# Performance work log

Hardware: AMD Instinct MI355X
Metric: run time of the kernel (lower is better)

## Reference

```python
import jax, jax.numpy as jnp
import numpy as np
from jax import lax

NEG = -10000.0
B, L, D = 256, 1024, 126  # batch, doc_len, d_output (tags); padded tagset T = D + 2


def setup_inputs() -> dict:
    key = jax.random.key(0)
    k1, k2, k3, k4 = jax.random.split(key, 4)
    x = jax.random.normal(k1, (B, L, D), dtype=jnp.float32)
    transitions = jax.random.normal(k2, (D + 2, D + 2), dtype=jnp.float32)
    x_len = jax.random.randint(k3, (B,), 1, L + 1, dtype=jnp.int32)
    x_mask = (jnp.arange(L)[None, :] < x_len[:, None]).astype(jnp.float32)
    true_tag = jax.random.randint(k4, (B, L), 0, D, dtype=jnp.int32)
    return {"x": x, "transitions": transitions, "x_mask": x_mask,
            "x_len": x_len, "true_tag": true_tag}


def _loglikelihood(x, transitions, x_mask, x_len, true_tag):
    b, l, d = x.shape
    T = transitions.shape[0]
    START, STOP = T - 2, T - 1
    # pad emissions with two impossible tags (START/STOP)
    logits = jnp.concatenate([x, jnp.full((b, l, 2), NEG, x.dtype)], axis=2)  # [B,L,T]

    # ---- partition function (forward algorithm, log-sum-exp scan) ----
    alpha0 = jnp.full((b, T), NEG, x.dtype).at[:, START].set(0.0)

    def step(alpha, inp):
        logit, m = inp  # [B,T], [B]
        # mat[b,i,j] = trans[i,j] + alpha[b,j] + logit[b,i]
        mat = transitions[None, :, :] + alpha[:, None, :] + logit[:, :, None]
        new = jax.nn.logsumexp(mat, axis=2)  # [B,T]
        m = m[:, None]
        return m * new + (1.0 - m) * alpha, None

    alpha, _ = lax.scan(step, alpha0, (jnp.swapaxes(logits, 0, 1), x_mask.T))
    partition = jax.nn.logsumexp(alpha + transitions[STOP][None, :], axis=1)  # [B]

    # ---- gold sequence score ----
    tag = true_tag.astype(jnp.int32)
    emission = jnp.take_along_axis(logits, tag[:, :, None], axis=2)[:, :, 0]
    emission = jnp.sum(emission * x_mask, axis=1)  # [B]

    tran = transitions[tag[:, 0], START]  # START -> first tag
    pair = transitions[tag[:, 1:], tag[:, :-1]] * x_mask[:, 1:]  # trans[next, prev]
    tran = tran + jnp.sum(pair, axis=1)
    last_tag = jnp.take_along_axis(tag, (x_len.astype(jnp.int32) - 1)[:, None], axis=1)[:, 0]
    tran = tran + transitions[STOP, last_tag]

    return tran + emission - partition  # [B]


def reference(x, transitions, x_mask, x_len, true_tag):
    return _loglikelihood(x, transitions, x_mask, x_len, true_tag)
```

## Files before the change

### kernel.cpp

```cpp
#include <hip/hip_runtime.h>


typedef float v2f __attribute__((ext_vector_type(2)));

#define NEGV  (-10000.0f)
#define LOG2E 1.4426950408889634f
#define LN2   0.6931471805599453f

constexpr int Bc = 256, Lc = 1024, Dc = 126, Tc = 128;

#if __has_builtin(__builtin_amdgcn_exp2f)
#define FEXP2(x) __builtin_amdgcn_exp2f(x)
#else
#define FEXP2(x) exp2f(x)
#endif
#if __has_builtin(__builtin_amdgcn_logf)
#define FLOG2(x) __builtin_amdgcn_logf(x)
#else
#define FLOG2(x) log2f(x)
#endif

#if __has_builtin(__builtin_amdgcn_mov_dpp)
#define DPPF(x, ctrl) __int_as_float(__builtin_amdgcn_mov_dpp(__float_as_int(x), (ctrl), 0xF, 0xF, true))
#define ROR1(x) DPPF(x, 0x121)
#define ROR2(x) DPPF(x, 0x122)
#define ROR4(x) DPPF(x, 0x124)
#define ROR8(x) DPPF(x, 0x128)
#else
#define ROR1(x) __shfl_xor((x), 1, 64)
#define ROR2(x) __shfl_xor((x), 2, 64)
#define ROR4(x) __shfl_xor((x), 4, 64)
#define ROR8(x) __shfl_xor((x), 8, 64)
#endif

#define STEP_BARRIER() asm volatile("s_waitcnt lgkmcnt(0)\n\ts_barrier" ::: "memory")

__device__ __forceinline__ int SIG(int q) { return q ^ (q >> 3); }
__device__ __forceinline__ int Fmap(int k) { return 4 * SIG(k >> 2) + (k & 3); }

__global__ __launch_bounds__(512, 1) void crf_fwd_kernel(
    const float* __restrict__ x,
    const float* __restrict__ trans,
    const int*   __restrict__ x_len,
    const int*   __restrict__ tag,
    float*       __restrict__ out)
{
    __shared__ __align__(16) float E[2][Tc];
    __shared__ float red[12];

    const int b   = blockIdx.x;
    const int tid = threadIdx.x;
    const int w   = tid >> 6;
    const int l6  = tid & 63;
    const int o   = l6 & 15;
    const int jg  = (w << 2) | (l6 >> 4);
    const int len = x_len[b];

    const float* xb = x   + (size_t)b * Lc * Dc;
    const int*   tb = tag + (size_t)b * Lc;

    const int  f0 = 4 * SIG(2 * o);
    const int  f1 = 4 * SIG(2 * o + 1);
    const int  wq = 4 * SIG(jg);
    const bool hiBad = (jg == 31);

    float treg[4][8];
#pragma unroll
    for (int g = 0; g < 4; ++g) {
        const float4* tp = reinterpret_cast<const float4*>(trans + (4*jg + g) * Tc + 8*o);
        float4 t0 = tp[0], t1 = tp[1];
        treg[g][0] = FEXP2(t0.x * LOG2E); treg[g][1] = FEXP2(t0.y * LOG2E);
        treg[g][2] = FEXP2(t0.z * LOG2E); treg[g][3] = FEXP2(t0.w * LOG2E);
        treg[g][4] = FEXP2(t1.x * LOG2E); treg[g][5] = FEXP2(t1.y * LOG2E);
        treg[g][6] = FEXP2(t1.z * LOG2E); treg[g][7] = FEXP2(t1.w * LOG2E);
    }

    if (tid < Tc) E[0][Fmap(tid)] = (tid == Tc - 2) ? 1.0f : 0.0f;
    __syncthreads();

#define LOADP(LS, A, B2) {                                              \
        int _s = (LS); if (_s > len - 1) _s = len - 1;                  \
        const float* _r = xb + (size_t)_s * Dc + 4 * jg;                \
        A  = *reinterpret_cast<const v2f*>(_r);                         \
        B2 = hiBad ? (v2f){NEGV, NEGV}                                  \
                   : *reinterpret_cast<const v2f*>(_r + 2); }

    v2f Pa, Pb;
    {
        v2f a, b2; LOADP(0, a, b2);
        Pa = (v2f){FEXP2(a.x * LOG2E),  FEXP2(a.y * LOG2E)};
        Pb = (v2f){FEXP2(b2.x * LOG2E), FEXP2(b2.y * LOG2E)};
    }
    v2f pA0, pB0, pA1, pB1, pA2, pB2, pA3, pB3;
    LOADP(1, pA1, pB1); LOADP(2, pA2, pB2); LOADP(3, pA3, pB3);
    pA0 = pA1; pB0 = pB1;

    int Mint = 0;
    const int len4 = (len + 3) & ~3;

#define BODY(C, PA_LD, PB_LD, PA_NX, PB_NX) {                                   \
        const int  l   = l4 + (C);                                              \
        const bool act = l < len;                 \
        const int  p   = (C) & 1;                                               \
        LOADP(l + 4, PA_LD, PB_LD);           \
        const float* Ep = E[p];                                                 \
        float4 ea = *reinterpret_cast<const float4*>(Ep + f0);                  \
        float4 eb = *reinterpret_cast<const float4*>(Ep + f1);                  \
        float a0 = treg[0][0]*ea.x, a1 = treg[1][0]*ea.x,                       \
              a2 = treg[2][0]*ea.x, a3 = treg[3][0]*ea.x;                       \
        a0=fmaf(treg[0][1],ea.y,a0); a1=fmaf(treg[1][1],ea.y,a1);               \
        a2=fmaf(treg[2][1],ea.y,a2); a3=fmaf(treg[3][1],ea.y,a3);               \
        a0=fmaf(treg[0][2],ea.z,a0); a1=fmaf(treg[1][2],ea.z,a1);               \
        a2=fmaf(treg[2][2],ea.z,a2); a3=fmaf(treg[3][2],ea.z,a3);               \
        a0=fmaf(treg[0][3],ea.w,a0); a1=fmaf(treg[1][3],ea.w,a1);               \
        a2=fmaf(treg[2][3],ea.w,a2); a3=fmaf(treg[3][3],ea.w,a3);               \
        a0=fmaf(treg[0][4],eb.x,a0); a1=fmaf(treg[1][4],eb.x,a1);               \
        a2=fmaf(treg[2][4],eb.x,a2); a3=fmaf(treg[3][4],eb.x,a3);               \
        a0=fmaf(treg[0][5],eb.y,a0); a1=fmaf(treg[1][5],eb.y,a1);               \
        a2=fmaf(treg[2][5],eb.y,a2); a3=fmaf(treg[3][5],eb.y,a3);               \
        a0=fmaf(treg[0][6],eb.z,a0); a1=fmaf(treg[1][6],eb.z,a1);               \
        a2=fmaf(treg[2][6],eb.z,a2); a3=fmaf(treg[3][6],eb.z,a3);               \
        a0=fmaf(treg[0][7],eb.w,a0); a1=fmaf(treg[1][7],eb.w,a1);               \
        a2=fmaf(treg[2][7],eb.w,a2); a3=fmaf(treg[3][7],eb.w,a3);               \
        a0 += ROR1(a0); a1 += ROR1(a1); a2 += ROR1(a2); a3 += ROR1(a3);         \
        a0 += ROR2(a0); a1 += ROR2(a1); a2 += ROR2(a2); a3 += ROR2(a3);         \
        a0 += ROR4(a0); a1 += ROR4(a1); a2 += ROR4(a2); a3 += ROR4(a3);         \
        a0 += ROR8(a0); a1 += ROR8(a1); a2 += ROR8(a2); a3 += ROR8(a3);         \
        float R = 1.0f;                                                         \
        if ((C) == 3 && act) {               \
            float mx = fmaxf(ea.z, eb.z);                                       \
            mx = fmaxf(mx, ROR1(mx)); mx = fmaxf(mx, ROR2(mx));                 \
            mx = fmaxf(mx, ROR4(mx)); mx = fmaxf(mx, ROR8(mx));                 \
            int ebq = (__float_as_int(mx) >> 23) & 0xFF;                        \
            R = __int_as_float((254 - ebq) << 23);                              \
            Mint += ebq - 127;                                                  \
        }                                                                       \
        if (act && o == 0)                 \
            *reinterpret_cast<float4*>(&E[p ^ 1][wq]) =                         \
                make_float4(a0 * Pa.x * R, a1 * Pa.y * R,                       \
                            a2 * Pb.x * R, a3 * Pb.y * R);                      \
        Pa = (v2f){FEXP2(PA_NX.x * LOG2E), FEXP2(PA_NX.y * LOG2E)};             \
        Pb = (v2f){FEXP2(PB_NX.x * LOG2E), FEXP2(PB_NX.y * LOG2E)};             \
        STEP_BARRIER();                                                         \
    }

    for (int l4 = 0; l4 < len4; l4 += 4) {
        BODY(0, pA0, pB0, pA1, pB1)
        BODY(1, pA1, pB1, pA2, pB2)
        BODY(2, pA2, pB2, pA3, pB3)
        BODY(3, pA3, pB3, pA0, pB0)
    }
#undef BODY
#undef LOADP
    const int pf = len & 1;

    float acc = 0.f;
    for (int l = tid; l < len; l += 512) {
        int   tg = tb[l];
        float tr = (l == 0) ? trans[tg * Tc + (Tc - 2)]
                            : trans[tg * Tc + tb[l - 1]];
        acc += xb[(size_t)l * Dc + tg] + tr;
    }
#pragma unroll
    for (int off = 1; off < 64; off <<= 1)
        acc += __shfl_xor(acc, off, 64);
    if (l6 == 0) red[w] = acc;

    if (w == 0) {
        int k0i = l6, k1i = 64 + l6;
        float p0 = FEXP2(trans[(Tc-1) * Tc + k0i] * LOG2E) * E[pf][Fmap(k0i)];
        float p1 = FEXP2(trans[(Tc-1) * Tc + k1i] * LOG2E) * E[pf][Fmap(k1i)];
        float ps = p0 + p1;
#pragma unroll
        for (int off = 1; off < 64; off <<= 1)
            ps += __shfl_xor(ps, off, 64);
        if (l6 == 0) red[8] = LN2 * ((float)Mint + FLOG2(ps));
    }
    __syncthreads();

    if (tid == 0) {
        float sc = trans[(Tc-1) * Tc + tb[len - 1]];
#pragma unroll
        for (int i = 0; i < 8; ++i) sc += red[i];
        out[b] = sc - red[8];
    }
}

extern "C" void kernel_launch(void* const* d_in, const int* in_sizes, int n_in,
                              void* d_out, int out_size, void* d_ws, size_t ws_size,
                              hipStream_t stream) {
    const float* x     = (const float*)d_in[0];
    const float* trans = (const float*)d_in[1];
    const int*   x_len = (const int*)d_in[3];
    const int*   tag   = (const int*)d_in[4];
    float*       out   = (float*)d_out;

    crf_fwd_kernel<<<Bc, 512, 0, stream>>>(x, trans, x_len, tag, out);
}
```

Measured before the change: 545.4 us.

## Process two batch sequences per block to share barriers and halve grid

Each block now runs the forward recursion for two batch elements at once, interleaving their matrix-vector products, ring reductions and emission loads so a single barrier per step serves both. The goal is to amortise the per-step barrier and LDS latency, which dominate the serial recurrence, across twice the independent work. The grid drops to 128 blocks, fewer than the CU count on MI355X, and each block iterates up to the longer of its two lengths, so idle CUs and length imbalance could offset the gain.

New measurement: 864.4 us. +58.5%, slower.

```diff
diff --git a/kernel.cpp b/kernel.cpp
--- a/kernel.cpp
+++ b/kernel.cpp
@@ -45,19 +45,23 @@
     const int*   __restrict__ tag,
     float*       __restrict__ out)
 {
-    __shared__ __align__(16) float E[2][Tc];
-    __shared__ float red[12];
-
-    const int b   = blockIdx.x;
+    __shared__ __align__(16) float EL[2][2][Tc];
+    __shared__ float red[2][12];
+
+    const int bb  = blockIdx.x << 1;
     const int tid = threadIdx.x;
     const int w   = tid >> 6;
     const int l6  = tid & 63;
     const int o   = l6 & 15;
     const int jg  = (w << 2) | (l6 >> 4);
-    const int len = x_len[b];
-
-    const float* xb = x   + (size_t)b * Lc * Dc;
-    const int*   tb = tag + (size_t)b * Lc;
+    const int len0 = x_len[bb];
+    const int len1 = x_len[bb + 1];
+    const int lenmax = (len0 > len1) ? len0 : len1;
+
+    const float* xb0 = x + (size_t)bb * Lc * Dc;
+    const float* xb1 = xb0 + (size_t)Lc * Dc;
+    const int*   tb0 = tag + (size_t)bb * Lc;
+    const int*   tb1 = tb0 + Lc;
 
     const int  f0 = 4 * SIG(2 * o);
     const int  f1 = 4 * SIG(2 * o + 1);
@@ -75,114 +79,163 @@
         treg[g][6] = FEXP2(t1.z * LOG2E); treg[g][7] = FEXP2(t1.w * LOG2E);
     }
 
-    if (tid < Tc) E[0][Fmap(tid)] = (tid == Tc - 2) ? 1.0f : 0.0f;
+    if (tid < Tc) {
+        float v = (tid == Tc - 2) ? 1.0f : 0.0f;
+        EL[0][0][Fmap(tid)] = v;
+        EL[1][0][Fmap(tid)] = v;
+    }
     __syncthreads();
 
-#define LOADP(LS, A, B2) {                                              \
-        int _s = (LS); if (_s > len - 1) _s = len - 1;                  \
-        const float* _r = xb + (size_t)_s * Dc + 4 * jg;                \
+#define LOADP(Q, LS, A, B2) {                                           \
+        int _s = (LS); const int _lm = len##Q - 1; if (_s > _lm) _s = _lm; \
+        const float* _r = xb##Q + (size_t)_s * Dc + 4 * jg;             \
         A  = *reinterpret_cast<const v2f*>(_r);                         \
         B2 = hiBad ? (v2f){NEGV, NEGV}                                  \
                    : *reinterpret_cast<const v2f*>(_r + 2); }
 
-    v2f Pa, Pb;
+    v2f Pa0, Pb0, Pa1, Pb1;
     {
-        v2f a, b2; LOADP(0, a, b2);
-        Pa = (v2f){FEXP2(a.x * LOG2E),  FEXP2(a.y * LOG2E)};
-        Pb = (v2f){FEXP2(b2.x * LOG2E), FEXP2(b2.y * LOG2E)};
-    }
-    v2f pA0, pB0, pA1, pB1, pA2, pB2, pA3, pB3;
-    LOADP(1, pA1, pB1); LOADP(2, pA2, pB2); LOADP(3, pA3, pB3);
-    pA0 = pA1; pB0 = pB1;
-
-    int Mint = 0;
-    const int len4 = (len + 3) & ~3;
-
-#define BODY(C, PA_LD, PB_LD, PA_NX, PB_NX) {                                   \
-        const int  l   = l4 + (C);                                              \
-        const bool act = l < len;                 \
-        const int  p   = (C) & 1;                                               \
-        LOADP(l + 4, PA_LD, PB_LD);           \
-        const float* Ep = E[p];                                                 \
-        float4 ea = *reinterpret_cast<const float4*>(Ep + f0);                  \
-        float4 eb = *reinterpret_cast<const float4*>(Ep + f1);                  \
-        float a0 = treg[0][0]*ea.x, a1 = treg[1][0]*ea.x,                       \
-              a2 = treg[2][0]*ea.x, a3 = treg[3][0]*ea.x;                       \
-        a0=fmaf(treg[0][1],ea.y,a0); a1=fmaf(treg[1][1],ea.y,a1);               \
-        a2=fmaf(treg[2][1],ea.y,a2); a3=fmaf(treg[3][1],ea.y,a3);               \
-        a0=fmaf(treg[0][2],ea.z,a0); a1=fmaf(treg[1][2],ea.z,a1);               \
-        a2=fmaf(treg[2][2],ea.z,a2); a3=fmaf(treg[3][2],ea.z,a3);               \
-        a0=fmaf(treg[0][3],ea.w,a0); a1=fmaf(treg[1][3],ea.w,a1);               \
-        a2=fmaf(treg[2][3],ea.w,a2); a3=fmaf(treg[3][3],ea.w,a3);               \
-        a0=fmaf(treg[0][4],eb.x,a0); a1=fmaf(treg[1][4],eb.x,a1);               \
-        a2=fmaf(treg[2][4],eb.x,a2); a3=fmaf(treg[3][4],eb.x,a3);               \
-        a0=fmaf(treg[0][5],eb.y,a0); a1=fmaf(treg[1][5],eb.y,a1);               \
-        a2=fmaf(treg[2][5],eb.y,a2); a3=fmaf(treg[3][5],eb.y,a3);               \
-        a0=fmaf(treg[0][6],eb.z,a0); a1=fmaf(treg[1][6],eb.z,a1);               \
-        a2=fmaf(treg[2][6],eb.z,a2); a3=fmaf(treg[3][6],eb.z,a3);               \
-        a0=fmaf(treg[0][7],eb.w,a0); a1=fmaf(treg[1][7],eb.w,a1);               \
-        a2=fmaf(treg[2][7],eb.w,a2); a3=fmaf(treg[3][7],eb.w,a3);               \
-        a0 += ROR1(a0); a1 += ROR1(a1); a2 += ROR1(a2); a3 += ROR1(a3);         \
-        a0 += ROR2(a0); a1 += ROR2(a1); a2 += ROR2(a2); a3 += ROR2(a3);         \
-        a0 += ROR4(a0); a1 += ROR4(a1); a2 += ROR4(a2); a3 += ROR4(a3);         \
-        a0 += ROR8(a0); a1 += ROR8(a1); a2 += ROR8(a2); a3 += ROR8(a3);         \
-        float R = 1.0f;                                                         \
-        if ((C) == 3 && act) {               \
-            float mx = fmaxf(ea.z, eb.z);                                       \
-            mx = fmaxf(mx, ROR1(mx)); mx = fmaxf(mx, ROR2(mx));                 \
-            mx = fmaxf(mx, ROR4(mx)); mx = fmaxf(mx, ROR8(mx));                 \
-            int ebq = (__float_as_int(mx) >> 23) & 0xFF;                        \
-            R = __int_as_float((254 - ebq) << 23);                              \
-            Mint += ebq - 127;                                                  \
+        v2f a, b2;
+        LOADP(0, 0, a, b2);
+        Pa0 = (v2f){FEXP2(a.x * LOG2E),  FEXP2(a.y * LOG2E)};
+        Pb0 = (v2f){FEXP2(b2.x * LOG2E), FEXP2(b2.y * LOG2E)};
+        LOADP(1, 0, a, b2);
+        Pa1 = (v2f){FEXP2(a.x * LOG2E),  FEXP2(a.y * LOG2E)};
+        Pb1 = (v2f){FEXP2(b2.x * LOG2E), FEXP2(b2.y * LOG2E)};
+    }
+    v2f s0A0,s0B0,s0A1,s0B1, s1A0,s1B0,s1A1,s1B1,
+        s2A0,s2B0,s2A1,s2B1, s3A0,s3B0,s3A1,s3B1;
+    LOADP(0, 1, s1A0, s1B0); LOADP(1, 1, s1A1, s1B1);
+    LOADP(0, 2, s2A0, s2B0); LOADP(1, 2, s2A1, s2B1);
+    LOADP(0, 3, s3A0, s3B0); LOADP(1, 3, s3A1, s3B1);
+    s0A0 = s1A0; s0B0 = s1B0; s0A1 = s1A1; s0B1 = s1B1;
+
+    int Mint0 = 0, Mint1 = 0;
+    const int len4 = (lenmax + 3) & ~3;
+
+#define MV32(ea, eb, S0, S1, S2, S3)                                                      \
+    S0 = treg[0][0]*ea.x; S1 = treg[1][0]*ea.x; S2 = treg[2][0]*ea.x; S3 = treg[3][0]*ea.x; \
+    S0=fmaf(treg[0][1],ea.y,S0); S1=fmaf(treg[1][1],ea.y,S1); S2=fmaf(treg[2][1],ea.y,S2); S3=fmaf(treg[3][1],ea.y,S3); \
+    S0=fmaf(treg[0][2],ea.z,S0); S1=fmaf(treg[1][2],ea.z,S1); S2=fmaf(treg[2][2],ea.z,S2); S3=fmaf(treg[3][2],ea.z,S3); \
+    S0=fmaf(treg[0][3],ea.w,S0); S1=fmaf(treg[1][3],ea.w,S1); S2=fmaf(treg[2][3],ea.w,S2); S3=fmaf(treg[3][3],ea.w,S3); \
+    S0=fmaf(treg[0][4],eb.x,S0); S1=fmaf(treg[1][4],eb.x,S1); S2=fmaf(treg[2][4],eb.x,S2); S3=fmaf(treg[3][4],eb.x,S3); \
+    S0=fmaf(treg[0][5],eb.y,S0); S1=fmaf(treg[1][5],eb.y,S1); S2=fmaf(treg[2][5],eb.y,S2); S3=fmaf(treg[3][5],eb.y,S3); \
+    S0=fmaf(treg[0][6],eb.z,S0); S1=fmaf(treg[1][6],eb.z,S1); S2=fmaf(treg[2][6],eb.z,S2); S3=fmaf(treg[3][6],eb.z,S3); \
+    S0=fmaf(treg[0][7],eb.w,S0); S1=fmaf(treg[1][7],eb.w,S1); S2=fmaf(treg[2][7],eb.w,S2); S3=fmaf(treg[3][7],eb.w,S3);
+
+#define RINGADD(S0, S1, S2, S3)                                     \
+    S0 += ROR1(S0); S1 += ROR1(S1); S2 += ROR1(S2); S3 += ROR1(S3); \
+    S0 += ROR2(S0); S1 += ROR2(S1); S2 += ROR2(S2); S3 += ROR2(S3); \
+    S0 += ROR4(S0); S1 += ROR4(S1); S2 += ROR4(S2); S3 += ROR4(S3); \
+    S0 += ROR8(S0); S1 += ROR8(S1); S2 += ROR8(S2); S3 += ROR8(S3);
+
+#define RINGMAX(M)                                                  \
+    M = fmaxf(M, ROR1(M)); M = fmaxf(M, ROR2(M));                   \
+    M = fmaxf(M, ROR4(M)); M = fmaxf(M, ROR8(M));
+
+#define BODY(C, L0A, L0B, N0A, N0B, L1A, L1B, N1A, N1B) {                       \
+        const int  l    = l4 + (C);                                             \
+        const bool act0 = l < len0, act1 = l < len1;         \
+        const int  p    = (C) & 1;                                              \
+        LOADP(0, l + 4, L0A, L0B);              \
+        LOADP(1, l + 4, L1A, L1B);                                              \
+        const float* Ep0 = EL[0][p];                                            \
+        const float* Ep1 = EL[1][p];                                            \
+        float4 ea0 = *reinterpret_cast<const float4*>(Ep0 + f0);                \
+        float4 eb0 = *reinterpret_cast<const float4*>(Ep0 + f1);                \
+        float4 ea1 = *reinterpret_cast<const float4*>(Ep1 + f0);                \
+        float4 eb1 = *reinterpret_cast<const float4*>(Ep1 + f1);                \
+        float x0, x1, x2, x3, y0, y1, y2, y3;                                   \
+        MV32(ea0, eb0, x0, x1, x2, x3);                                         \
+        MV32(ea1, eb1, y0, y1, y2, y3);                                         \
+        RINGADD(x0, x1, x2, x3);                                                \
+        RINGADD(y0, y1, y2, y3);                                                \
+        float R0 = 1.0f, R1 = 1.0f;                                             \
+        if ((C) == 3) {                      \
+            if (act0) {                                                         \
+                float mx = fmaxf(ea0.z, eb0.z); RINGMAX(mx);                    \
+                int e = (__float_as_int(mx) >> 23) & 0xFF;                      \
+                R0 = __int_as_float((254 - e) << 23); Mint0 += e - 127;         \
+            }                                                                   \
+            if (act1) {                                                         \
+                float mx = fmaxf(ea1.z, eb1.z); RINGMAX(mx);                    \
+                int e = (__float_as_int(mx) >> 23) & 0xFF;                      \
+                R1 = __int_as_float((254 - e) << 23); Mint1 += e - 127;         \
+            }                                                                   \
         }                                                                       \
-        if (act && o == 0)                 \
-            *reinterpret_cast<float4*>(&E[p ^ 1][wq]) =                         \
-                make_float4(a0 * Pa.x * R, a1 * Pa.y * R,                       \
-                            a2 * Pb.x * R, a3 * Pb.y * R);                      \
-        Pa = (v2f){FEXP2(PA_NX.x * LOG2E), FEXP2(PA_NX.y * LOG2E)};             \
-        Pb = (v2f){FEXP2(PB_NX.x * LOG2E), FEXP2(PB_NX.y * LOG2E)};             \
+        if (o == 0) {                        \
+            if (act0) *reinterpret_cast<float4*>(&EL[0][p ^ 1][wq]) =           \
+                make_float4(x0 * Pa0.x * R0, x1 * Pa0.y * R0,                   \
+                            x2 * Pb0.x * R0, x3 * Pb0.y * R0);                  \
+            if (act1) *reinterpret_cast<float4*>(&EL[1][p ^ 1][wq]) =           \
+                make_float4(y0 * Pa1.x * R1, y1 * Pa1.y * R1,                   \
+                            y2 * Pb1.x * R1, y3 * Pb1.y * R1);                  \
+        }                                                                       \
+        Pa0 = (v2f){FEXP2(N0A.x * LOG2E), FEXP2(N0A.y * LOG2E)};                \
+        Pb0 = (v2f){FEXP2(N0B.x * LOG2E), FEXP2(N0B.y * LOG2E)};                \
+        Pa1 = (v2f){FEXP2(N1A.x * LOG2E), FEXP2(N1A.y * LOG2E)};                \
+        Pb1 = (v2f){FEXP2(N1B.x * LOG2E), FEXP2(N1B.y * LOG2E)};                \
         STEP_BARRIER();                                                         \
     }
 
     for (int l4 = 0; l4 < len4; l4 += 4) {
-        BODY(0, pA0, pB0, pA1, pB1)
-        BODY(1, pA1, pB1, pA2, pB2)
-        BODY(2, pA2, pB2, pA3, pB3)
-        BODY(3, pA3, pB3, pA0, pB0)
+        BODY(0, s0A0,s0B0, s1A0,s1B0,  s0A1,s0B1, s1A1,s1B1)
+        BODY(1, s1A0,s1B0, s2A0,s2B0,  s1A1,s1B1, s2A1,s2B1)
+        BODY(2, s2A0,s2B0, s3A0,s3B0,  s2A1,s2B1, s3A1,s3B1)
+        BODY(3, s3A0,s3B0, s0A0,s0B0,  s3A1,s3B1, s0A1,s0B1)
     }
 #undef BODY
 #undef LOADP
-    const int pf = len & 1;
-
-    float acc = 0.f;
-    for (int l = tid; l < len; l += 512) {
-        int   tg = tb[l];
+    const int pf0 = len0 & 1, pf1 = len1 & 1;
+
+    float acc0 = 0.f, acc1 = 0.f;
+    for (int l = tid; l < len0; l += 512) {
+        int   tg = tb0[l];
         float tr = (l == 0) ? trans[tg * Tc + (Tc - 2)]
-                            : trans[tg * Tc + tb[l - 1]];
-        acc += xb[(size_t)l * Dc + tg] + tr;
-    }
-#pragma unroll
-    for (int off = 1; off < 64; off <<= 1)
-        acc += __shfl_xor(acc, off, 64);
-    if (l6 == 0) red[w] = acc;
+                            : trans[tg * Tc + tb0[l - 1]];
+        acc0 += xb0[(size_t)l * Dc + tg] + tr;
+    }
+    for (int l = tid; l < len1; l += 512) {
+        int   tg = tb1[l];
+        float tr = (l == 0) ? trans[tg * Tc + (Tc - 2)]
+                            : trans[tg * Tc + tb1[l - 1]];
+        acc1 += xb1[(size_t)l * Dc + tg] + tr;
+    }
+#pragma unroll
+    for (int off = 1; off < 64; off <<= 1) {
+        acc0 += __shfl_xor(acc0, off, 64);
+        acc1 += __shfl_xor(acc1, off, 64);
+    }
+    if (l6 == 0) { red[0][w] = acc0; red[1][w] = acc1; }
 
     if (w == 0) {
         int k0i = l6, k1i = 64 + l6;
-        float p0 = FEXP2(trans[(Tc-1) * Tc + k0i] * LOG2E) * E[pf][Fmap(k0i)];
-        float p1 = FEXP2(trans[(Tc-1) * Tc + k1i] * LOG2E) * E[pf][Fmap(k1i)];
+        float p0 = FEXP2(trans[(Tc-1) * Tc + k0i] * LOG2E) * EL[0][pf0][Fmap(k0i)];
+        float p1 = FEXP2(trans[(Tc-1) * Tc + k1i] * LOG2E) * EL[0][pf0][Fmap(k1i)];
         float ps = p0 + p1;
 #pragma unroll
         for (int off = 1; off < 64; off <<= 1)
             ps += __shfl_xor(ps, off, 64);
-        if (l6 == 0) red[8] = LN2 * ((float)Mint + FLOG2(ps));
+        if (l6 == 0) red[0][8] = LN2 * ((float)Mint0 + FLOG2(ps));
+    } else if (w == 1) {
+        int k0i = l6, k1i = 64 + l6;
+        float p0 = FEXP2(trans[(Tc-1) * Tc + k0i] * LOG2E) * EL[1][pf1][Fmap(k0i)];
+        float p1 = FEXP2(trans[(Tc-1) * Tc + k1i] * LOG2E) * EL[1][pf1][Fmap(k1i)];
+        float ps = p0 + p1;
+#pragma unroll
+        for (int off = 1; off < 64; off <<= 1)
+            ps += __shfl_xor(ps, off, 64);
+        if (l6 == 0) red[1][8] = LN2 * ((float)Mint1 + FLOG2(ps));
     }
     __syncthreads();
 
     if (tid == 0) {
-        float sc = trans[(Tc-1) * Tc + tb[len - 1]];
-#pragma unroll
-        for (int i = 0; i < 8; ++i) sc += red[i];
-        out[b] = sc - red[8];
+        float sc0 = trans[(Tc-1) * Tc + tb0[len0 - 1]];
+        float sc1 = trans[(Tc-1) * Tc + tb1[len1 - 1]];
+#pragma unroll
+        for (int i = 0; i < 8; ++i) { sc0 += red[0][i]; sc1 += red[1][i]; }
+        out[bb]     = sc0 - red[0][8];
+        out[bb + 1] = sc1 - red[1][8];
     }
 }
 
@@ -195,5 +248,5 @@
     const int*   tag   = (const int*)d_in[4];
     float*       out   = (float*)d_out;
 
-    crf_fwd_kernel<<<Bc, 512, 0, stream>>>(x, trans, x_len, tag, out);
+    crf_fwd_kernel<<<Bc / 2, 512, 0, stream>>>(x, trans, x_len, tag, out);
 }
```

## Shrink CRF forward block to 128 threads with 8-lane reductions and 128 transition registers

Applied to the files above, without the earlier changes.

The block drops from 512 to 128 threads (two waves), so each step's barrier spans fewer waves. Each thread now keeps 8 rows by 16 columns of exp(transitions) in registers, and the lane reduction shrinks from four DPP stages to three (quad xor and half-mirror). Each thread then selects and writes a single new alpha entry. Per-thread FMA work per step grows and register pressure rises to about 128 floats, but barrier cost and cross-lane reduction depth fall. The LDS swizzle changes accordingly.

New measurement: 707.7 us. 1.3x slower.

```diff
diff --git a/kernel.cpp b/kernel.cpp
--- a/kernel.cpp
+++ b/kernel.cpp
@@ -1,7 +1,5 @@
 #include <hip/hip_runtime.h>
 
-
-typedef float v2f __attribute__((ext_vector_type(2)));
 
 #define NEGV  (-10000.0f)
 #define LOG2E 1.4426950408889634f
@@ -22,23 +20,21 @@
 
 #if __has_builtin(__builtin_amdgcn_mov_dpp)
 #define DPPF(x, ctrl) __int_as_float(__builtin_amdgcn_mov_dpp(__float_as_int(x), (ctrl), 0xF, 0xF, true))
-#define ROR1(x) DPPF(x, 0x121)
-#define ROR2(x) DPPF(x, 0x122)
-#define ROR4(x) DPPF(x, 0x124)
-#define ROR8(x) DPPF(x, 0x128)
+#define QX1(x)  DPPF(x, 0xB1)
+#define QX2(x)  DPPF(x, 0x4E)
+#define HMIR(x) DPPF(x, 0x141)
 #else
-#define ROR1(x) __shfl_xor((x), 1, 64)
-#define ROR2(x) __shfl_xor((x), 2, 64)
-#define ROR4(x) __shfl_xor((x), 4, 64)
-#define ROR8(x) __shfl_xor((x), 8, 64)
+#define QX1(x)  __shfl_xor((x), 1, 64)
+#define QX2(x)  __shfl_xor((x), 2, 64)
+#define HMIR(x) __shfl_xor((x), 4, 64)
 #endif
 
 #define STEP_BARRIER() asm volatile("s_waitcnt lgkmcnt(0)\n\ts_barrier" ::: "memory")
 
-__device__ __forceinline__ int SIG(int q) { return q ^ (q >> 3); }
-__device__ __forceinline__ int Fmap(int k) { return 4 * SIG(k >> 2) + (k & 3); }
-
-__global__ __launch_bounds__(512, 1) void crf_fwd_kernel(
+__device__ __forceinline__ int PI(int q) { return q ^ (q >> 2); }
+__device__ __forceinline__ int Fmap(int k) { return 4 * PI(k >> 2) + (k & 3); }
+
+__global__ __launch_bounds__(128, 1) void crf_fwd_kernel(
     const float* __restrict__ x,
     const float* __restrict__ trans,
     const int*   __restrict__ x_len,
@@ -46,116 +42,128 @@
     float*       __restrict__ out)
 {
     __shared__ __align__(16) float E[2][Tc];
-    __shared__ float red[12];
+    __shared__ float red[4];
 
     const int b   = blockIdx.x;
     const int tid = threadIdx.x;
     const int w   = tid >> 6;
     const int l6  = tid & 63;
-    const int o   = l6 & 15;
-    const int jg  = (w << 2) | (l6 >> 4);
+    const int o   = l6 & 7;
+    const int jb  = (tid >> 3) << 3;
     const int len = x_len[b];
 
     const float* xb = x   + (size_t)b * Lc * Dc;
     const int*   tb = tag + (size_t)b * Lc;
 
-    const int  f0 = 4 * SIG(2 * o);
-    const int  f1 = 4 * SIG(2 * o + 1);
-    const int  wq = 4 * SIG(jg);
-    const bool hiBad = (jg == 31);
-
-    float treg[4][8];
-#pragma unroll
-    for (int g = 0; g < 4; ++g) {
-        const float4* tp = reinterpret_cast<const float4*>(trans + (4*jg + g) * Tc + 8*o);
-        float4 t0 = tp[0], t1 = tp[1];
-        treg[g][0] = FEXP2(t0.x * LOG2E); treg[g][1] = FEXP2(t0.y * LOG2E);
-        treg[g][2] = FEXP2(t0.z * LOG2E); treg[g][3] = FEXP2(t0.w * LOG2E);
-        treg[g][4] = FEXP2(t1.x * LOG2E); treg[g][5] = FEXP2(t1.y * LOG2E);
-        treg[g][6] = FEXP2(t1.z * LOG2E); treg[g][7] = FEXP2(t1.w * LOG2E);
-    }
-
-    if (tid < Tc) E[0][Fmap(tid)] = (tid == Tc - 2) ? 1.0f : 0.0f;
+    const bool jOK = tid < Dc;
+
+    const int f0 = 4 * PI(4 * o + 0);
+    const int f1 = 4 * PI(4 * o + 1);
+    const int f2 = 4 * PI(4 * o + 2);
+    const int f3 = 4 * PI(4 * o + 3);
+    const int widx = Fmap(tid);
+
+    float treg[8][16];
+#pragma unroll
+    for (int s = 0; s < 8; ++s) {
+        const float4* tp = reinterpret_cast<const float4*>(trans + (jb + s) * Tc + (o << 4));
+#pragma unroll
+        for (int c4 = 0; c4 < 4; ++c4) {
+            float4 t4 = tp[c4];
+            treg[s][4*c4+0] = FEXP2(t4.x * LOG2E);
+            treg[s][4*c4+1] = FEXP2(t4.y * LOG2E);
+            treg[s][4*c4+2] = FEXP2(t4.z * LOG2E);
+            treg[s][4*c4+3] = FEXP2(t4.w * LOG2E);
+        }
+    }
+
+    E[0][widx] = (tid == Tc - 2) ? 1.0f : 0.0f;
     __syncthreads();
 
-#define LOADP(LS, A, B2) {                                              \
-        int _s = (LS); if (_s > len - 1) _s = len - 1;                  \
-        const float* _r = xb + (size_t)_s * Dc + 4 * jg;                \
-        A  = *reinterpret_cast<const v2f*>(_r);                         \
-        B2 = hiBad ? (v2f){NEGV, NEGV}                                  \
-                   : *reinterpret_cast<const v2f*>(_r + 2); }
-
-    v2f Pa, Pb;
-    {
-        v2f a, b2; LOADP(0, a, b2);
-        Pa = (v2f){FEXP2(a.x * LOG2E),  FEXP2(a.y * LOG2E)};
-        Pb = (v2f){FEXP2(b2.x * LOG2E), FEXP2(b2.y * LOG2E)};
-    }
-    v2f pA0, pB0, pA1, pB1, pA2, pB2, pA3, pB3;
-    LOADP(1, pA1, pB1); LOADP(2, pA2, pB2); LOADP(3, pA3, pB3);
-    pA0 = pA1; pB0 = pB1;
+#define LOADL(LS, DST) {                                        \
+        int _s = (LS); if (_s > len - 1) _s = len - 1;          \
+        DST = jOK ? xb[(size_t)_s * Dc + tid] : NEGV; }
+
+    float P;
+    { float l0; LOADL(0, l0); P = jOK ? FEXP2(l0 * LOG2E) : 0.0f; }
+    float q0, q1, q2, q3;
+    LOADL(1, q1); LOADL(2, q2); LOADL(3, q3);
+    q0 = q1;
 
     int Mint = 0;
     const int len4 = (len + 3) & ~3;
 
-#define BODY(C, PA_LD, PB_LD, PA_NX, PB_NX) {                                   \
+#define BODY(C, QL, QN) {                                                       \
         const int  l   = l4 + (C);                                              \
         const bool act = l < len;                 \
         const int  p   = (C) & 1;                                               \
-        LOADP(l + 4, PA_LD, PB_LD);           \
+        LOADL(l + 4, QL);                       \
         const float* Ep = E[p];                                                 \
-        float4 ea = *reinterpret_cast<const float4*>(Ep + f0);                  \
-        float4 eb = *reinterpret_cast<const float4*>(Ep + f1);                  \
-        float a0 = treg[0][0]*ea.x, a1 = treg[1][0]*ea.x,                       \
-              a2 = treg[2][0]*ea.x, a3 = treg[3][0]*ea.x;                       \
-        a0=fmaf(treg[0][1],ea.y,a0); a1=fmaf(treg[1][1],ea.y,a1);               \
-        a2=fmaf(treg[2][1],ea.y,a2); a3=fmaf(treg[3][1],ea.y,a3);               \
-        a0=fmaf(treg[0][2],ea.z,a0); a1=fmaf(treg[1][2],ea.z,a1);               \
-        a2=fmaf(treg[2][2],ea.z,a2); a3=fmaf(treg[3][2],ea.z,a3);               \
-        a0=fmaf(treg[0][3],ea.w,a0); a1=fmaf(treg[1][3],ea.w,a1);               \
-        a2=fmaf(treg[2][3],ea.w,a2); a3=fmaf(treg[3][3],ea.w,a3);               \
-        a0=fmaf(treg[0][4],eb.x,a0); a1=fmaf(treg[1][4],eb.x,a1);               \
-        a2=fmaf(treg[2][4],eb.x,a2); a3=fmaf(treg[3][4],eb.x,a3);               \
-        a0=fmaf(treg[0][5],eb.y,a0); a1=fmaf(treg[1][5],eb.y,a1);               \
-        a2=fmaf(treg[2][5],eb.y,a2); a3=fmaf(treg[3][5],eb.y,a3);               \
-        a0=fmaf(treg[0][6],eb.z,a0); a1=fmaf(treg[1][6],eb.z,a1);               \
-        a2=fmaf(treg[2][6],eb.z,a2); a3=fmaf(treg[3][6],eb.z,a3);               \
-        a0=fmaf(treg[0][7],eb.w,a0); a1=fmaf(treg[1][7],eb.w,a1);               \
-        a2=fmaf(treg[2][7],eb.w,a2); a3=fmaf(treg[3][7],eb.w,a3);               \
-        a0 += ROR1(a0); a1 += ROR1(a1); a2 += ROR1(a2); a3 += ROR1(a3);         \
-        a0 += ROR2(a0); a1 += ROR2(a1); a2 += ROR2(a2); a3 += ROR2(a3);         \
-        a0 += ROR4(a0); a1 += ROR4(a1); a2 += ROR4(a2); a3 += ROR4(a3);         \
-        a0 += ROR8(a0); a1 += ROR8(a1); a2 += ROR8(a2); a3 += ROR8(a3);         \
+        float4 e0 = *reinterpret_cast<const float4*>(Ep + f0);                  \
+        float4 e1 = *reinterpret_cast<const float4*>(Ep + f1);                  \
+        float4 e2 = *reinterpret_cast<const float4*>(Ep + f2);                  \
+        float4 e3 = *reinterpret_cast<const float4*>(Ep + f3);                  \
+        float acc[8];                                                           \
+        _Pragma("unroll")                                                       \
+        for (int s = 0; s < 8; ++s) {           \
+            float a = treg[s][0] * e0.x;                                        \
+            a = fmaf(treg[s][1],  e0.y, a);                                     \
+            a = fmaf(treg[s][2],  e0.z, a);                                     \
+            a = fmaf(treg[s][3],  e0.w, a);                                     \
+            a = fmaf(treg[s][4],  e1.x, a);                                     \
+            a = fmaf(treg[s][5],  e1.y, a);                                     \
+            a = fmaf(treg[s][6],  e1.z, a);                                     \
+            a = fmaf(treg[s][7],  e1.w, a);                                     \
+            a = fmaf(treg[s][8],  e2.x, a);                                     \
+            a = fmaf(treg[s][9],  e2.y, a);                                     \
+            a = fmaf(treg[s][10], e2.z, a);                                     \
+            a = fmaf(treg[s][11], e2.w, a);                                     \
+            a = fmaf(treg[s][12], e3.x, a);                                     \
+            a = fmaf(treg[s][13], e3.y, a);                                     \
+            a = fmaf(treg[s][14], e3.z, a);                                     \
+            a = fmaf(treg[s][15], e3.w, a);                                     \
+            acc[s] = a;                                                         \
+        }                                                                       \
+        _Pragma("unroll")                                                       \
+        for (int s = 0; s < 8; ++s) acc[s] += QX1(acc[s]);                      \
+        _Pragma("unroll")                                                       \
+        for (int s = 0; s < 8; ++s) acc[s] += QX2(acc[s]);                      \
+        _Pragma("unroll")                                                       \
+        for (int s = 0; s < 8; ++s) acc[s] += HMIR(acc[s]);                     \
         float R = 1.0f;                                                         \
         if ((C) == 3 && act) {               \
-            float mx = fmaxf(ea.z, eb.z);                                       \
-            mx = fmaxf(mx, ROR1(mx)); mx = fmaxf(mx, ROR2(mx));                 \
-            mx = fmaxf(mx, ROR4(mx)); mx = fmaxf(mx, ROR8(mx));                 \
+            float mx = fmaxf(fmaxf(e0.z, e1.z), fmaxf(e2.z, e3.z));             \
+            mx = fmaxf(mx, QX1(mx)); mx = fmaxf(mx, QX2(mx));                   \
+            mx = fmaxf(mx, HMIR(mx));                                           \
             int ebq = (__float_as_int(mx) >> 23) & 0xFF;                        \
             R = __int_as_float((254 - ebq) << 23);                              \
             Mint += ebq - 127;                                                  \
         }                                                                       \
-        if (act && o == 0)                 \
-            *reinterpret_cast<float4*>(&E[p ^ 1][wq]) =                         \
-                make_float4(a0 * Pa.x * R, a1 * Pa.y * R,                       \
-                            a2 * Pb.x * R, a3 * Pb.y * R);                      \
-        Pa = (v2f){FEXP2(PA_NX.x * LOG2E), FEXP2(PA_NX.y * LOG2E)};             \
-        Pb = (v2f){FEXP2(PB_NX.x * LOG2E), FEXP2(PB_NX.y * LOG2E)};             \
+           \
+        float sA = (o & 1) ? acc[1] : acc[0];                                   \
+        float sB = (o & 1) ? acc[3] : acc[2];                                   \
+        float sC = (o & 1) ? acc[5] : acc[4];                                   \
+        float sD = (o & 1) ? acc[7] : acc[6];                                   \
+        float sE = (o & 2) ? sB : sA;                                           \
+        float sF = (o & 2) ? sD : sC;                                           \
+        float sel = (o & 4) ? sF : sE;                                          \
+        if (act) E[p ^ 1][widx] = sel * P * R;                                  \
+        P = jOK ? FEXP2(QN * LOG2E) : 0.0f;                                     \
         STEP_BARRIER();                                                         \
     }
 
     for (int l4 = 0; l4 < len4; l4 += 4) {
-        BODY(0, pA0, pB0, pA1, pB1)
-        BODY(1, pA1, pB1, pA2, pB2)
-        BODY(2, pA2, pB2, pA3, pB3)
-        BODY(3, pA3, pB3, pA0, pB0)
+        BODY(0, q0, q1)
+        BODY(1, q1, q2)
+        BODY(2, q2, q3)
+        BODY(3, q3, q0)
     }
 #undef BODY
-#undef LOADP
+#undef LOADL
     const int pf = len & 1;
 
     float acc = 0.f;
-    for (int l = tid; l < len; l += 512) {
+    for (int l = tid; l < len; l += 128) {
         int   tg = tb[l];
         float tr = (l == 0) ? trans[tg * Tc + (Tc - 2)]
                             : trans[tg * Tc + tb[l - 1]];
@@ -174,15 +182,13 @@
 #pragma unroll
         for (int off = 1; off < 64; off <<= 1)
             ps += __shfl_xor(ps, off, 64);
-        if (l6 == 0) red[8] = LN2 * ((float)Mint + FLOG2(ps));
+        if (l6 == 0) red[2] = LN2 * ((float)Mint + FLOG2(ps));
     }
     __syncthreads();
 
     if (tid == 0) {
-        float sc = trans[(Tc-1) * Tc + tb[len - 1]];
-#pragma unroll
-        for (int i = 0; i < 8; ++i) sc += red[i];
-        out[b] = sc - red[8];
+        float sc = red[0] + red[1] + trans[(Tc-1) * Tc + tb[len - 1]];
+        out[b] = sc - red[2];
     }
 }
 
@@ -195,5 +201,5 @@
     const int*   tag   = (const int*)d_in[4];
     float*       out   = (float*)d_out;
 
-    crf_fwd_kernel<<<Bc, 512, 0, stream>>>(x, trans, x_len, tag, out);
+    crf_fwd_kernel<<<Bc, 128, 0, stream>>>(x, trans, x_len, tag, out);
 }
```
